# Optimization experiments

Measured on AMD Instinct MI355X. Metric: run time of the kernel, lower is better.

The kernel has to match this reference:

```python
import jax, jax.numpy as jnp
import numpy as np

NUM_USERS = 8000
NUM_ITEMS = 4000
EMB_DIM = 64
NUM_LAYERS = 3
NUM_EDGES = 300000
N = NUM_USERS + NUM_ITEMS


def setup_inputs() -> dict:
    key = jax.random.key(0)
    k1, k2, k3 = jax.random.split(key, 3)
    edge_index = jax.random.randint(k1, (2, NUM_EDGES), 0, N, dtype=jnp.int64 if jax.config.jax_enable_x64 else jnp.int32)
    # xavier-uniform-like init
    bound = float(np.sqrt(6.0 / (NUM_USERS + EMB_DIM)))
    user_emb = jax.random.uniform(k2, (NUM_USERS, EMB_DIM), jnp.float32, -bound, bound)
    bound_i = float(np.sqrt(6.0 / (NUM_ITEMS + EMB_DIM)))
    item_emb = jax.random.uniform(k3, (NUM_ITEMS, EMB_DIM), jnp.float32, -bound_i, bound_i)
    return {"edge_index": edge_index, "user_emb": user_emb, "item_emb": item_emb}


def _normalized_adj(edge_index):
    # dense symmetric adjacency from edge list, then D^{-1/2} A D^{-1/2}
    adj = jnp.zeros((N, N), jnp.float32)
    adj = adj.at[edge_index[0], edge_index[1]].set(1.0)
    adj = adj.at[edge_index[1], edge_index[0]].set(1.0)
    degree = jnp.clip(adj.sum(axis=1, keepdims=True), 1.0)  # (N,1)
    dsqrt = jnp.sqrt(degree)
    return adj / dsqrt / dsqrt.T


def reference(edge_index, user_emb, item_emb):
    adj = _normalized_adj(edge_index)
    all_emb = jnp.concatenate([user_emb, item_emb], axis=0)  # (N, d)
    acc = all_emb
    cur = all_emb
    for _ in range(NUM_LAYERS):
        cur = adj @ cur
        acc = acc + cur
    final = acc / (NUM_LAYERS + 1)  # mean over layer outputs
    return final[:NUM_USERS], final[NUM_USERS:]
```

## Files before the change

### kernel.cpp

```cpp
#include <hip/hip_runtime.h>
#include <hip/hip_bf16.h>

namespace {

constexpr int NU = 8000;
constexpr int NI = 4000;
constexpr int NN = 12000;
constexpr int D  = 64;
constexpr int NE = 300000;
constexpr int STRIDE = 128;

__device__ __forceinline__ int probe_e32(const unsigned* raw, int lane) {
    unsigned v = raw[2 * lane + 1];
    return (__ballot(v != 0u) != 0ull) ? 1 : 0;
}
__device__ __forceinline__ int probe_f32(const unsigned short* ue, int lane) {
    int e = (ue[2 * lane] >> 7) & 0xFF;
    return (__ballot(e > 126) != 0ull) ? 1 : 0;
}

__global__ __launch_bounds__(256) void scatter_init(const unsigned* __restrict__ raw,
                                                    const unsigned short* __restrict__ ue,
                                                    const unsigned short* __restrict__ ie,
                                                    unsigned* __restrict__ fill,
                                                    int* __restrict__ col,
                                                    unsigned short* __restrict__ x0,
                                                    unsigned short* __restrict__ x1,
                                                    float* __restrict__ out) {
    const int tid  = blockIdx.x * blockDim.x + threadIdx.x;
    const int NT   = gridDim.x * blockDim.x;
    const int lane = threadIdx.x & 63;
    const int e32  = probe_e32(raw, lane);
    const int f32  = probe_f32(ue, lane);
    const unsigned base = fill[NN];

    for (int t2 = tid; t2 < NE / 2; t2 += NT) {
        int a0, b0, a1, b1;
        if (e32) {
            uint2 av = *(const uint2*)(raw + 2 * t2);
            uint2 bv = *(const uint2*)(raw + NE + 2 * t2);
            a0 = (int)av.x; a1 = (int)av.y;
            b0 = (int)bv.x; b1 = (int)bv.y;
        } else {
            uint4 av = *(const uint4*)(raw + 4 * t2);
            uint4 bv = *(const uint4*)(raw + 2 * NE + 4 * t2);
            a0 = (int)av.x; a1 = (int)av.z;
            b0 = (int)bv.x; b1 = (int)bv.z;
        }
        unsigned s = atomicAdd(&fill[a0], 1u) - base;
        if (s < STRIDE) col[a0 * STRIDE + s] = b0;
        if (a0 != b0) {
            s = atomicAdd(&fill[b0], 1u) - base;
            if (s < STRIDE) col[b0 * STRIDE + s] = a0;
        }
        s = atomicAdd(&fill[a1], 1u) - base;
        if (s < STRIDE) col[a1 * STRIDE + s] = b1;
        if (a1 != b1) {
            s = atomicAdd(&fill[b1], 1u) - base;
            if (s < STRIDE) col[b1 * STRIDE + s] = a1;
        }
    }
    for (int q = tid; q < NN * D / 4; q += NT) {
        int i = q * 4;
        float4 vf;
        ushort4 vb;
        if (f32) {
            const float* src = (i < NU * D) ? ((const float*)ue) + i
                                            : ((const float*)ie) + (i - NU * D);
            vf = *(const float4*)src;
            vb.x = __bfloat16_as_ushort(__float2bfloat16(vf.x));
            vb.y = __bfloat16_as_ushort(__float2bfloat16(vf.y));
            vb.z = __bfloat16_as_ushort(__float2bfloat16(vf.z));
            vb.w = __bfloat16_as_ushort(__float2bfloat16(vf.w));
        } else {
            const unsigned short* src = (i < NU * D) ? ue + i : ie + (i - NU * D);
            vb = *(const ushort4*)src;
            vf.x = __uint_as_float(((unsigned)vb.x) << 16);
            vf.y = __uint_as_float(((unsigned)vb.y) << 16);
            vf.z = __uint_as_float(((unsigned)vb.z) << 16);
            vf.w = __uint_as_float(((unsigned)vb.w) << 16);
        }
        *(ushort4*)(x0 + i) = vb;
        *(float4*)(out + i) = vf;
    }
    if (tid < D / 4) {
        *(ushort4*)(x0 + NN * D + 4 * tid) = make_ushort4(0, 0, 0, 0);
        *(ushort4*)(x1 + NN * D + 4 * tid) = make_ushort4(0, 0, 0, 0);
    }
}

__global__ __launch_bounds__(256) void dedup(const unsigned* __restrict__ fill,
                                             int* __restrict__ col,
                                             float* __restrict__ dinv,
                                             unsigned short* __restrict__ x0) {
    __shared__ unsigned bits[4][376];
    __shared__ int cnt[4];
    const int lane = threadIdx.x & 63;
    const int wave = __builtin_amdgcn_readfirstlane(threadIdx.x >> 6);
    const int row  = blockIdx.x * 4 + wave;
    unsigned* bb = bits[wave];
    for (int w = lane; w < 376; w += 64) bb[w] = 0;
    if (lane == 0) cnt[wave] = 0;
    const unsigned base = fill[NN];
    unsigned nn = fill[row] - base;
    int n = (int)(nn < (unsigned)STRIDE ? nn : (unsigned)STRIDE);
    const int cbase = row * STRIDE;
    for (int cb = 0; cb < n; cb += 64) {
        int idx = cb + lane;
        if (idx < n) {
            int c = col[cbase + idx];
            unsigned bit = 1u << (c & 31);
            unsigned old = atomicOr(&bb[c >> 5], bit);
            if (!(old & bit)) {
                int pos = atomicAdd(&cnt[wave], 1);
                col[cbase + pos] = c;
            }
        }
    }
    int d = cnt[wave];
    int n8 = (d + 7) & ~7;
    if (lane < n8 - d) col[cbase + d + lane] = NN;
    float dr = rsqrtf((float)(d > 0 ? d : 1));
    if (lane == 0) dinv[row] = dr;
    const int o = row * D + lane;
    float v = __uint_as_float(((unsigned)x0[o]) << 16);
    x0[o] = __bfloat16_as_ushort(__float2bfloat16(dr * v));
}

__global__ __launch_bounds__(256) void spmm(const float* __restrict__ dinv,
                                            const int* __restrict__ col,
                                            const unsigned short* __restrict__ zin,
                                            unsigned short* __restrict__ zout,
                                            float* __restrict__ out,
                                            int final_layer) {
    const int lane = threadIdx.x & 63;
    const int wave = __builtin_amdgcn_readfirstlane(threadIdx.x >> 6);
    const int row  = blockIdx.x * 4 + wave;
    const int oct  = lane >> 3;
    const int sub  = lane & 7;
    const float dr = dinv[row];
    const int d  = (int)(1.0f / (dr * dr) + 0.5f);
    const int n8 = (d + 7) & ~7;
    const int base = row * STRIDE;
    float s0 = 0.f, s1 = 0.f, s2 = 0.f, s3 = 0.f;
    float s4 = 0.f, s5 = 0.f, s6 = 0.f, s7 = 0.f;
    #pragma unroll 4
    for (int j = 0; j < n8; j += 8) {
        int c = col[base + j + oct];
        uint4 u = *(const uint4*)(zin + c * D + 8 * sub);
        s0 += __uint_as_float(u.x << 16);
        s1 += __uint_as_float(u.x & 0xFFFF0000u);
        s2 += __uint_as_float(u.y << 16);
        s3 += __uint_as_float(u.y & 0xFFFF0000u);
        s4 += __uint_as_float(u.z << 16);
        s5 += __uint_as_float(u.z & 0xFFFF0000u);
        s6 += __uint_as_float(u.w << 16);
        s7 += __uint_as_float(u.w & 0xFFFF0000u);
    }
    #pragma unroll
    for (int m = 8; m <= 32; m <<= 1) {
        s0 += __shfl(s0, lane ^ m, 64);  s1 += __shfl(s1, lane ^ m, 64);
        s2 += __shfl(s2, lane ^ m, 64);  s3 += __shfl(s3, lane ^ m, 64);
        s4 += __shfl(s4, lane ^ m, 64);  s5 += __shfl(s5, lane ^ m, 64);
        s6 += __shfl(s6, lane ^ m, 64);  s7 += __shfl(s7, lane ^ m, 64);
    }
    if (lane < 8) {
        const int o = row * D + 8 * sub;
        float4 p0 = *(const float4*)(out + o);
        float4 p1 = *(const float4*)(out + o + 4);
        float y0 = dr * s0, y1 = dr * s1, y2 = dr * s2, y3 = dr * s3;
        float y4 = dr * s4, y5 = dr * s5, y6 = dr * s6, y7 = dr * s7;
        if (final_layer) {
            float4 r0, r1;
            r0.x = (p0.x + y0) * 0.25f;  r0.y = (p0.y + y1) * 0.25f;
            r0.z = (p0.z + y2) * 0.25f;  r0.w = (p0.w + y3) * 0.25f;
            r1.x = (p1.x + y4) * 0.25f;  r1.y = (p1.y + y5) * 0.25f;
            r1.z = (p1.z + y6) * 0.25f;  r1.w = (p1.w + y7) * 0.25f;
            *(float4*)(out + o)     = r0;
            *(float4*)(out + o + 4) = r1;
        } else {
            ushort4 z0, z1;
            z0.x = __bfloat16_as_ushort(__float2bfloat16(dr * y0));
            z0.y = __bfloat16_as_ushort(__float2bfloat16(dr * y1));
            z0.z = __bfloat16_as_ushort(__float2bfloat16(dr * y2));
            z0.w = __bfloat16_as_ushort(__float2bfloat16(dr * y3));
            z1.x = __bfloat16_as_ushort(__float2bfloat16(dr * y4));
            z1.y = __bfloat16_as_ushort(__float2bfloat16(dr * y5));
            z1.z = __bfloat16_as_ushort(__float2bfloat16(dr * y6));
            z1.w = __bfloat16_as_ushort(__float2bfloat16(dr * y7));
            *(ushort4*)(zout + o)     = z0;
            *(ushort4*)(zout + o + 4) = z1;
            float4 r0, r1;
            r0.x = p0.x + y0;  r0.y = p0.y + y1;
            r0.z = p0.z + y2;  r0.w = p0.w + y3;
            r1.x = p1.x + y4;  r1.y = p1.y + y5;
            r1.z = p1.z + y6;  r1.w = p1.w + y7;
            *(float4*)(out + o)     = r0;
            *(float4*)(out + o + 4) = r1;
        }
    }
}

}

extern "C" void kernel_launch(void* const* d_in, const int* in_sizes, int n_in,
                              void* d_out, int out_size, void* d_ws, size_t ws_size,
                              hipStream_t stream) {
    int ei = 0, ui = 1, ii = 2;
    for (int i = 0; i < n_in; ++i) {
        if      (in_sizes[i] == 2 * NE) ei = i;
        else if (in_sizes[i] == NU * D) ui = i;
        else if (in_sizes[i] == NI * D) ii = i;
    }
    const unsigned*       raw = (const unsigned*)d_in[ei];
    const unsigned short* ue  = (const unsigned short*)d_in[ui];
    const unsigned short* ie  = (const unsigned short*)d_in[ii];
    float*                out = (float*)d_out;

    char* ws = (char*)d_ws;
    size_t off = 0;
    auto take = [&](size_t bytes) {
        void* p = ws + off;
        off += (bytes + 15) & ~(size_t)15;
        return p;
    };
    unsigned*       fill = (unsigned*)take((NN + 1) * 4);
    float*          dinv = (float*)take(NN * 4);
    int*            col  = (int*)take((size_t)NN * STRIDE * 4);
    unsigned short* x0   = (unsigned short*)take((size_t)(NN + 1) * D * 2);
    unsigned short* x1   = (unsigned short*)take((size_t)(NN + 1) * D * 2);
    (void)ws_size;

    scatter_init<<<1024, 256, 0, stream>>>(raw, ue, ie, fill, col, x0, x1, out);
    dedup<<<NN / 4, 256, 0, stream>>>(fill, col, dinv, x0);

    spmm<<<NN / 4, 256, 0, stream>>>(dinv, col, x0, x1, out, 0);
    spmm<<<NN / 4, 256, 0, stream>>>(dinv, col, x1, x0, out, 0);
    spmm<<<NN / 4, 256, 0, stream>>>(dinv, col, x0, nullptr, out, 1);
}
```

Before: 133.7 us.

## Dedup edges via global hash and fuse three SpMM layers with grid barrier

Duplicate edges are now filtered during the scatter using a global open-addressing hash table with CAS, which removes the separate per-row dedup kernel. The three propagation layers are merged into one persistent kernel of 1024 blocks that synchronise through a software grid barrier, cutting launch overhead and inter-kernel gaps. The first layer applies the input-side degree scaling on the fly by reading neighbour fill counts, instead of pre-scaling x0. In exchange, the random CAS traffic on an 8 MB hash table adds cost, and the barrier is only safe if all 1024 blocks are co-resident on the GPU.

After: 394.7 us. +195.1%, slower.

```diff
diff --git a/kernel.cpp b/kernel.cpp
--- a/kernel.cpp
+++ b/kernel.cpp
@@ -10,6 +10,13 @@
 constexpr int NE = 300000;
 constexpr int STRIDE = 128;
 
+constexpr int HBITS = 21;
+constexpr int HSIZE = 1 << HBITS;
+constexpr unsigned HMASK = (unsigned)(HSIZE - 1);
+
+constexpr int SB = 1024;
+constexpr int SW = SB * 4;
+
 __device__ __forceinline__ int probe_e32(const unsigned* raw, int lane) {
     unsigned v = raw[2 * lane + 1];
     return (__ballot(v != 0u) != 0ull) ? 1 : 0;
@@ -17,22 +24,45 @@
 __device__ __forceinline__ int probe_f32(const unsigned short* ue, int lane) {
     int e = (ue[2 * lane] >> 7) & 0xFF;
     return (__ballot(e > 126) != 0ull) ? 1 : 0;
+}
+
+__device__ __forceinline__ void insert_edge(int a, int b, unsigned hbase, unsigned pbase,
+                                            unsigned* __restrict__ hash,
+                                            unsigned* __restrict__ fill,
+                                            int* __restrict__ col) {
+    const int mn = a < b ? a : b;
+    const int mx = a < b ? b : a;
+    const unsigned key = (((unsigned)mn << 14) | (unsigned)mx) + 1u;
+    unsigned h = (key * 2654435761u) >> (32 - HBITS);
+    for (;;) {
+        unsigned old = atomicCAS(&hash[h & HMASK], hbase, hbase ^ key);
+        if (old == hbase) break;
+        if (old == (hbase ^ key)) return;
+        ++h;
+    }
+    unsigned s = atomicAdd(&fill[a], 1u) - pbase;
+    if (s < STRIDE) col[a * STRIDE + s] = b;
+    if (a != b) {
+        s = atomicAdd(&fill[b], 1u) - pbase;
+        if (s < STRIDE) col[b * STRIDE + s] = a;
+    }
 }
 
 __global__ __launch_bounds__(256) void scatter_init(const unsigned* __restrict__ raw,
                                                     const unsigned short* __restrict__ ue,
                                                     const unsigned short* __restrict__ ie,
                                                     unsigned* __restrict__ fill,
+                                                    unsigned* __restrict__ hash,
                                                     int* __restrict__ col,
                                                     unsigned short* __restrict__ x0,
-                                                    unsigned short* __restrict__ x1,
                                                     float* __restrict__ out) {
     const int tid  = blockIdx.x * blockDim.x + threadIdx.x;
     const int NT   = gridDim.x * blockDim.x;
     const int lane = threadIdx.x & 63;
     const int e32  = probe_e32(raw, lane);
     const int f32  = probe_f32(ue, lane);
-    const unsigned base = fill[NN];
+    const unsigned pbase = fill[NN];
+    const unsigned hbase = hash[HSIZE];
 
     for (int t2 = tid; t2 < NE / 2; t2 += NT) {
         int a0, b0, a1, b1;
@@ -47,18 +77,8 @@
             a0 = (int)av.x; a1 = (int)av.z;
             b0 = (int)bv.x; b1 = (int)bv.z;
         }
-        unsigned s = atomicAdd(&fill[a0], 1u) - base;
-        if (s < STRIDE) col[a0 * STRIDE + s] = b0;
-        if (a0 != b0) {
-            s = atomicAdd(&fill[b0], 1u) - base;
-            if (s < STRIDE) col[b0 * STRIDE + s] = a0;
-        }
-        s = atomicAdd(&fill[a1], 1u) - base;
-        if (s < STRIDE) col[a1 * STRIDE + s] = b1;
-        if (a1 != b1) {
-            s = atomicAdd(&fill[b1], 1u) - base;
-            if (s < STRIDE) col[b1 * STRIDE + s] = a1;
-        }
+        insert_edge(a0, b0, hbase, pbase, hash, fill, col);
+        insert_edge(a1, b1, hbase, pbase, hash, fill, col);
     }
     for (int q = tid; q < NN * D / 4; q += NT) {
         int i = q * 4;
@@ -83,122 +103,132 @@
         *(ushort4*)(x0 + i) = vb;
         *(float4*)(out + i) = vf;
     }
-    if (tid < D / 4) {
-        *(ushort4*)(x0 + NN * D + 4 * tid) = make_ushort4(0, 0, 0, 0);
-        *(ushort4*)(x1 + NN * D + 4 * tid) = make_ushort4(0, 0, 0, 0);
-    }
-}
-
-__global__ __launch_bounds__(256) void dedup(const unsigned* __restrict__ fill,
-                                             int* __restrict__ col,
-                                             float* __restrict__ dinv,
-                                             unsigned short* __restrict__ x0) {
-    __shared__ unsigned bits[4][376];
-    __shared__ int cnt[4];
+}
+
+__device__ __forceinline__ void grid_barrier(unsigned* __restrict__ bar, unsigned bbase,
+                                             unsigned gbase, int phase) {
+    __syncthreads();
+    if (threadIdx.x == 0) {
+        unsigned old = __hip_atomic_fetch_add(&bar[0], 1u, __ATOMIC_ACQ_REL,
+                                              __HIP_MEMORY_SCOPE_AGENT);
+        if (old == bbase + (unsigned)SB - 1u) {
+            __hip_atomic_fetch_add(&bar[0], (unsigned)(0u - (unsigned)SB),
+                                   __ATOMIC_ACQ_REL, __HIP_MEMORY_SCOPE_AGENT);
+            __hip_atomic_fetch_add(&bar[16], 1u, __ATOMIC_ACQ_REL,
+                                   __HIP_MEMORY_SCOPE_AGENT);
+        } else {
+            while ((int)(__hip_atomic_load(&bar[16], __ATOMIC_ACQUIRE,
+                                           __HIP_MEMORY_SCOPE_AGENT) - gbase) <
+                   phase + 1) {
+                __builtin_amdgcn_s_sleep(2);
+            }
+        }
+    }
+    __syncthreads();
+}
+
+template <bool SCALE_IN, bool FINAL>
+__device__ __forceinline__ void spmm_layer(int wid, int oct, int sub, int lane,
+                                           unsigned pbase,
+                                           const unsigned* __restrict__ fill,
+                                           const int* __restrict__ col,
+                                           const unsigned short* __restrict__ zin,
+                                           unsigned short* __restrict__ zout,
+                                           float* __restrict__ out) {
+    for (int row = wid; row < NN; row += SW) {
+        int dd = (int)(fill[row] - pbase);
+        int d  = dd < STRIDE ? dd : STRIDE;
+        const float dr = rsqrtf((float)(d > 0 ? d : 1));
+        const int base = row * STRIDE;
+        float s0 = 0.f, s1 = 0.f, s2 = 0.f, s3 = 0.f;
+        float s4 = 0.f, s5 = 0.f, s6 = 0.f, s7 = 0.f;
+        #pragma unroll 4
+        for (int jj = oct; jj < d; jj += 8) {
+            int c = col[base + jj];
+            float w;
+            if (SCALE_IN) {
+                int dc = (int)(fill[c] - pbase);
+                w = rsqrtf((float)(dc > 0 ? dc : 1));
+            } else {
+                w = 1.0f;
+            }
+            uint4 u = *(const uint4*)(zin + c * D + 8 * sub);
+            s0 = fmaf(w, __uint_as_float(u.x << 16), s0);
+            s1 = fmaf(w, __uint_as_float(u.x & 0xFFFF0000u), s1);
+            s2 = fmaf(w, __uint_as_float(u.y << 16), s2);
+            s3 = fmaf(w, __uint_as_float(u.y & 0xFFFF0000u), s3);
+            s4 = fmaf(w, __uint_as_float(u.z << 16), s4);
+            s5 = fmaf(w, __uint_as_float(u.z & 0xFFFF0000u), s5);
+            s6 = fmaf(w, __uint_as_float(u.w << 16), s6);
+            s7 = fmaf(w, __uint_as_float(u.w & 0xFFFF0000u), s7);
+        }
+        #pragma unroll
+        for (int m = 8; m <= 32; m <<= 1) {
+            s0 += __shfl(s0, lane ^ m, 64);  s1 += __shfl(s1, lane ^ m, 64);
+            s2 += __shfl(s2, lane ^ m, 64);  s3 += __shfl(s3, lane ^ m, 64);
+            s4 += __shfl(s4, lane ^ m, 64);  s5 += __shfl(s5, lane ^ m, 64);
+            s6 += __shfl(s6, lane ^ m, 64);  s7 += __shfl(s7, lane ^ m, 64);
+        }
+        if (lane < 8) {
+            const int o = row * D + 8 * sub;
+            float4 p0 = *(const float4*)(out + o);
+            float4 p1 = *(const float4*)(out + o + 4);
+            float y0 = dr * s0, y1 = dr * s1, y2 = dr * s2, y3 = dr * s3;
+            float y4 = dr * s4, y5 = dr * s5, y6 = dr * s6, y7 = dr * s7;
+            if (FINAL) {
+                float4 r0, r1;
+                r0.x = (p0.x + y0) * 0.25f;  r0.y = (p0.y + y1) * 0.25f;
+                r0.z = (p0.z + y2) * 0.25f;  r0.w = (p0.w + y3) * 0.25f;
+                r1.x = (p1.x + y4) * 0.25f;  r1.y = (p1.y + y5) * 0.25f;
+                r1.z = (p1.z + y6) * 0.25f;  r1.w = (p1.w + y7) * 0.25f;
+                *(float4*)(out + o)     = r0;
+                *(float4*)(out + o + 4) = r1;
+            } else {
+                ushort4 z0, z1;
+                z0.x = __bfloat16_as_ushort(__float2bfloat16(dr * y0));
+                z0.y = __bfloat16_as_ushort(__float2bfloat16(dr * y1));
+                z0.z = __bfloat16_as_ushort(__float2bfloat16(dr * y2));
+                z0.w = __bfloat16_as_ushort(__float2bfloat16(dr * y3));
+                z1.x = __bfloat16_as_ushort(__float2bfloat16(dr * y4));
+                z1.y = __bfloat16_as_ushort(__float2bfloat16(dr * y5));
+                z1.z = __bfloat16_as_ushort(__float2bfloat16(dr * y6));
+                z1.w = __bfloat16_as_ushort(__float2bfloat16(dr * y7));
+                *(ushort4*)(zout + o)     = z0;
+                *(ushort4*)(zout + o + 4) = z1;
+                float4 r0, r1;
+                r0.x = p0.x + y0;  r0.y = p0.y + y1;
+                r0.z = p0.z + y2;  r0.w = p0.w + y3;
+                r1.x = p1.x + y4;  r1.y = p1.y + y5;
+                r1.z = p1.z + y6;  r1.w = p1.w + y7;
+                *(float4*)(out + o)     = r0;
+                *(float4*)(out + o + 4) = r1;
+            }
+        }
+    }
+}
+
+__global__ __launch_bounds__(256, 4) void spmm_fused(const unsigned* __restrict__ fill,
+                                                     const int* __restrict__ col,
+                                                     const unsigned short* __restrict__ x0,
+                                                     unsigned short* __restrict__ z1,
+                                                     unsigned short* __restrict__ z2,
+                                                     float* __restrict__ out,
+                                                     unsigned* __restrict__ bar) {
     const int lane = threadIdx.x & 63;
     const int wave = __builtin_amdgcn_readfirstlane(threadIdx.x >> 6);
-    const int row  = blockIdx.x * 4 + wave;
-    unsigned* bb = bits[wave];
-    for (int w = lane; w < 376; w += 64) bb[w] = 0;
-    if (lane == 0) cnt[wave] = 0;
-    const unsigned base = fill[NN];
-    unsigned nn = fill[row] - base;
-    int n = (int)(nn < (unsigned)STRIDE ? nn : (unsigned)STRIDE);
-    const int cbase = row * STRIDE;
-    for (int cb = 0; cb < n; cb += 64) {
-        int idx = cb + lane;
-        if (idx < n) {
-            int c = col[cbase + idx];
-            unsigned bit = 1u << (c & 31);
-            unsigned old = atomicOr(&bb[c >> 5], bit);
-            if (!(old & bit)) {
-                int pos = atomicAdd(&cnt[wave], 1);
-                col[cbase + pos] = c;
-            }
-        }
-    }
-    int d = cnt[wave];
-    int n8 = (d + 7) & ~7;
-    if (lane < n8 - d) col[cbase + d + lane] = NN;
-    float dr = rsqrtf((float)(d > 0 ? d : 1));
-    if (lane == 0) dinv[row] = dr;
-    const int o = row * D + lane;
-    float v = __uint_as_float(((unsigned)x0[o]) << 16);
-    x0[o] = __bfloat16_as_ushort(__float2bfloat16(dr * v));
-}
-
-__global__ __launch_bounds__(256) void spmm(const float* __restrict__ dinv,
-                                            const int* __restrict__ col,
-                                            const unsigned short* __restrict__ zin,
-                                            unsigned short* __restrict__ zout,
-                                            float* __restrict__ out,
-                                            int final_layer) {
-    const int lane = threadIdx.x & 63;
-    const int wave = __builtin_amdgcn_readfirstlane(threadIdx.x >> 6);
-    const int row  = blockIdx.x * 4 + wave;
+    const int wid  = blockIdx.x * 4 + wave;
     const int oct  = lane >> 3;
     const int sub  = lane & 7;
-    const float dr = dinv[row];
-    const int d  = (int)(1.0f / (dr * dr) + 0.5f);
-    const int n8 = (d + 7) & ~7;
-    const int base = row * STRIDE;
-    float s0 = 0.f, s1 = 0.f, s2 = 0.f, s3 = 0.f;
-    float s4 = 0.f, s5 = 0.f, s6 = 0.f, s7 = 0.f;
-    #pragma unroll 4
-    for (int j = 0; j < n8; j += 8) {
-        int c = col[base + j + oct];
-        uint4 u = *(const uint4*)(zin + c * D + 8 * sub);
-        s0 += __uint_as_float(u.x << 16);
-        s1 += __uint_as_float(u.x & 0xFFFF0000u);
-        s2 += __uint_as_float(u.y << 16);
-        s3 += __uint_as_float(u.y & 0xFFFF0000u);
-        s4 += __uint_as_float(u.z << 16);
-        s5 += __uint_as_float(u.z & 0xFFFF0000u);
-        s6 += __uint_as_float(u.w << 16);
-        s7 += __uint_as_float(u.w & 0xFFFF0000u);
-    }
-    #pragma unroll
-    for (int m = 8; m <= 32; m <<= 1) {
-        s0 += __shfl(s0, lane ^ m, 64);  s1 += __shfl(s1, lane ^ m, 64);
-        s2 += __shfl(s2, lane ^ m, 64);  s3 += __shfl(s3, lane ^ m, 64);
-        s4 += __shfl(s4, lane ^ m, 64);  s5 += __shfl(s5, lane ^ m, 64);
-        s6 += __shfl(s6, lane ^ m, 64);  s7 += __shfl(s7, lane ^ m, 64);
-    }
-    if (lane < 8) {
-        const int o = row * D + 8 * sub;
-        float4 p0 = *(const float4*)(out + o);
-        float4 p1 = *(const float4*)(out + o + 4);
-        float y0 = dr * s0, y1 = dr * s1, y2 = dr * s2, y3 = dr * s3;
-        float y4 = dr * s4, y5 = dr * s5, y6 = dr * s6, y7 = dr * s7;
-        if (final_layer) {
-            float4 r0, r1;
-            r0.x = (p0.x + y0) * 0.25f;  r0.y = (p0.y + y1) * 0.25f;
-            r0.z = (p0.z + y2) * 0.25f;  r0.w = (p0.w + y3) * 0.25f;
-            r1.x = (p1.x + y4) * 0.25f;  r1.y = (p1.y + y5) * 0.25f;
-            r1.z = (p1.z + y6) * 0.25f;  r1.w = (p1.w + y7) * 0.25f;
-            *(float4*)(out + o)     = r0;
-            *(float4*)(out + o + 4) = r1;
-        } else {
-            ushort4 z0, z1;
-            z0.x = __bfloat16_as_ushort(__float2bfloat16(dr * y0));
-            z0.y = __bfloat16_as_ushort(__float2bfloat16(dr * y1));
-            z0.z = __bfloat16_as_ushort(__float2bfloat16(dr * y2));
-            z0.w = __bfloat16_as_ushort(__float2bfloat16(dr * y3));
-            z1.x = __bfloat16_as_ushort(__float2bfloat16(dr * y4));
-            z1.y = __bfloat16_as_ushort(__float2bfloat16(dr * y5));
-            z1.z = __bfloat16_as_ushort(__float2bfloat16(dr * y6));
-            z1.w = __bfloat16_as_ushort(__float2bfloat16(dr * y7));
-            *(ushort4*)(zout + o)     = z0;
-            *(ushort4*)(zout + o + 4) = z1;
-            float4 r0, r1;
-            r0.x = p0.x + y0;  r0.y = p0.y + y1;
-            r0.z = p0.z + y2;  r0.w = p0.w + y3;
-            r1.x = p1.x + y4;  r1.y = p1.y + y5;
-            r1.z = p1.z + y6;  r1.w = p1.w + y7;
-            *(float4*)(out + o)     = r0;
-            *(float4*)(out + o + 4) = r1;
-        }
-    }
+    const unsigned pbase = fill[NN];
+    const unsigned bbase = bar[32];
+    const unsigned gbase = __hip_atomic_load(&bar[16], __ATOMIC_ACQUIRE,
+                                             __HIP_MEMORY_SCOPE_AGENT);
+
+    spmm_layer<true,  false>(wid, oct, sub, lane, pbase, fill, col, x0, z1, out);
+    grid_barrier(bar, bbase, gbase, 0);
+    spmm_layer<false, false>(wid, oct, sub, lane, pbase, fill, col, z1, z2, out);
+    grid_barrier(bar, bbase, gbase, 1);
+    spmm_layer<false, true >(wid, oct, sub, lane, pbase, fill, col, z2, nullptr, out);
 }
 
 }
@@ -221,20 +251,18 @@
     size_t off = 0;
     auto take = [&](size_t bytes) {
         void* p = ws + off;
-        off += (bytes + 15) & ~(size_t)15;
+        off += (bytes + 63) & ~(size_t)63;
         return p;
     };
     unsigned*       fill = (unsigned*)take((NN + 1) * 4);
-    float*          dinv = (float*)take(NN * 4);
+    unsigned*       bar  = (unsigned*)take(64 * 4);
     int*            col  = (int*)take((size_t)NN * STRIDE * 4);
-    unsigned short* x0   = (unsigned short*)take((size_t)(NN + 1) * D * 2);
-    unsigned short* x1   = (unsigned short*)take((size_t)(NN + 1) * D * 2);
+    unsigned short* x0   = (unsigned short*)take((size_t)NN * D * 2);
+    unsigned short* z1   = (unsigned short*)take((size_t)NN * D * 2);
+    unsigned short* z2   = (unsigned short*)take((size_t)NN * D * 2);
+    unsigned*       hash = (unsigned*)take(((size_t)HSIZE + 1) * 4);
     (void)ws_size;
 
-    scatter_init<<<1024, 256, 0, stream>>>(raw, ue, ie, fill, col, x0, x1, out);
-    dedup<<<NN / 4, 256, 0, stream>>>(fill, col, dinv, x0);
-
-    spmm<<<NN / 4, 256, 0, stream>>>(dinv, col, x0, x1, out, 0);
-    spmm<<<NN / 4, 256, 0, stream>>>(dinv, col, x1, x0, out, 0);
-    spmm<<<NN / 4, 256, 0, stream>>>(dinv, col, x0, nullptr, out, 1);
-}
+    scatter_init<<<1024, 256, 0, stream>>>(raw, ue, ie, fill, hash, col, x0, out);
+    spmm_fused<<<SB, 256, 0, stream>>>(fill, col, x0, z1, z2, out, bar);
+}
```
